# Kernel tuning notes

Hardware: AMD Instinct MI355X
Metric: run time of the kernel (lower is better)

Reference implementation:

```python
import jax, jax.numpy as jnp
import numpy as np

F_DIM = 128
RBF_DIM = 20
N_NODES = 10000
N_EDGES = 200000
CUTOFF = 5


def setup_inputs() -> dict:
    key = jax.random.key(0)
    ks = jax.random.split(key, 12)
    s = jax.random.normal(ks[0], (N_NODES, F_DIM), jnp.float32)
    vec = jax.random.normal(ks[1], (N_NODES, 3, F_DIM), jnp.float32)
    edge_indexes = jax.random.randint(ks[2], (2, N_EDGES), 0, N_NODES, jnp.int32)
    edge_vector = jax.random.normal(ks[3], (N_EDGES, 3), jnp.float32)
    # distances in (0.5, 5.0) so fcut is nontrivial and no divide-by-zero
    edge_distance = jax.random.uniform(ks[4], (N_EDGES,), jnp.float32) * 4.5 + 0.5
    edge_rbf = jax.random.normal(ks[5], (N_EDGES, RBF_DIM), jnp.float32)
    # params: linear_s = Linear(F,F) -> SiLU -> Linear(F,3F); linear_rbf = Linear(RBF,3F)
    Ws1 = jax.random.normal(ks[6], (F_DIM, F_DIM), jnp.float32) / np.sqrt(F_DIM)
    bs1 = jnp.zeros((F_DIM,), jnp.float32)
    Ws2 = jax.random.normal(ks[7], (3 * F_DIM, F_DIM), jnp.float32) / np.sqrt(F_DIM)
    bs2 = jnp.zeros((3 * F_DIM,), jnp.float32)
    Wrbf = jax.random.normal(ks[8], (3 * F_DIM, RBF_DIM), jnp.float32) / np.sqrt(RBF_DIM)
    brbf = jnp.zeros((3 * F_DIM,), jnp.float32)
    return {
        "s": s, "vec": vec, "edge_vector": edge_vector,
        "edge_distance": edge_distance, "edge_rbf": edge_rbf,
        "Ws1": Ws1, "bs1": bs1, "Ws2": Ws2, "bs2": bs2,
        "Wrbf": Wrbf, "brbf": brbf,
        "edge_indexes": edge_indexes, "cutoff_dist": CUTOFF,
    }


def reference(s, vec, edge_vector, edge_distance, edge_rbf,
              Ws1, bs1, Ws2, bs2, Wrbf, brbf,
              edge_indexes, cutoff_dist):
    num_atoms, nf = s.shape
    dst_recv = edge_indexes[0]   # index_add target (message receivers)
    src_send = edge_indexes[1]   # gather source (message senders)

    S = s[src_send]              # [E, F]
    Vec = vec[src_send]          # [E, 3, F]

    # linear_s: Linear -> SiLU -> Linear
    h = jax.nn.silu(S @ Ws1.T + bs1)          # [E, F]
    phi = h @ Ws2.T + bs2                      # [E, 3F]

    rbf_lin = edge_rbf @ Wrbf.T + brbf         # [E, 3F]
    # cosine cutoff: 0.5*(cos(pi*d/rc)+1) for d < rc else 0
    rc = jnp.asarray(cutoff_dist, edge_distance.dtype)
    fcut = 0.5 * (jnp.cos(jnp.pi * edge_distance / rc) + 1.0)
    fcut = jnp.where(edge_distance < rc, fcut, 0.0)

    W = rbf_lin * fcut[:, None]
    vec_Ws, vec_Wvv, vec_Wvs = jnp.split(phi * W, 3, axis=-1)  # each [E, F]

    ds = jnp.zeros((num_atoms, nf), s.dtype).at[dst_recv].add(vec_Ws)

    vec_n = edge_vector / edge_distance[:, None]               # [E, 3]
    dVec = vec_Wvv[:, None, :] * Vec + vec_n[:, :, None] * vec_Wvs[:, None, :]  # [E,3,F]
    dvec = jnp.zeros((num_atoms, 3, nf), s.dtype).at[dst_recv].add(dVec)

    return ds, dvec
```

## Files before the change

kernel.cpp:

```cpp
#include <hip/hip_runtime.h>
#include <hip/hip_bf16.h>

typedef __attribute__((ext_vector_type(8))) short short8;
typedef __attribute__((ext_vector_type(4))) float floatx4;
typedef _Float16 half2_t __attribute__((ext_vector_type(2)));

#define CAP 64

__device__ __forceinline__ unsigned short f2bf(float x) {
    unsigned u = __float_as_uint(x);
    unsigned r = u + 0x7fffu + ((u >> 16) & 1u);
    return (unsigned short)(r >> 16);
}
__device__ __forceinline__ float bf2f(unsigned short h) {
    return __uint_as_float(((unsigned)h) << 16);
}
__device__ __forceinline__ unsigned short f2h(float x) {
    _Float16 h = (_Float16)x;
    return __builtin_bit_cast(unsigned short, h);
}
__device__ __forceinline__ float FD(unsigned int a, unsigned int b, float c) {
#if __has_builtin(__builtin_amdgcn_fdot2)
    return __builtin_amdgcn_fdot2(__builtin_bit_cast(half2_t, a),
                                  __builtin_bit_cast(half2_t, b), c, false);
#else
    half2_t ha = __builtin_bit_cast(half2_t, a);
    half2_t hb = __builtin_bit_cast(half2_t, b);
    return c + (float)ha[0] * (float)hb[0] + (float)ha[1] * (float)hb[1];
#endif
}
__device__ __forceinline__ float decode_rc(const void* cutoff_raw) {
    float fv = ((const float*)cutoff_raw)[0];
    int   iv = ((const int*)cutoff_raw)[0];
    if (fv > 0.099f && fv < 1.0e6f) return fv;
    if (iv > 0 && iv < 1000000) return (float)iv;
    double dv = ((const double*)cutoff_raw)[0];
    if (dv > 0.099 && dv < 1.0e6) return (float)dv;
    return (float)(((const long long*)cutoff_raw)[0]);
}

__global__ void setup_kernel(const float* __restrict__ vec,
                             const float* __restrict__ Ws1,
                             const float* __restrict__ Ws2,
                             const float* __restrict__ Wrbf,
                             const float* __restrict__ edge_rbf,
                             const int* __restrict__ eidx,
                             const float* __restrict__ edge_vec,
                             const float* __restrict__ edge_dist,
                             const void* __restrict__ cutoff_raw,
                             unsigned short* __restrict__ P6,
                             unsigned short* __restrict__ ws1_bf,
                             unsigned short* __restrict__ ws2_bf,
                             unsigned short* __restrict__ wrbf_h,
                             unsigned short* __restrict__ rbf_h,
                             int* __restrict__ cnt,
                             unsigned int* __restrict__ rec,
                             int ng_vec, int ng_w1, int ng_w2, int ng_wh, int ng_rh,
                             int RB, int E, int nbc)
{
    int tid = threadIdx.x;
    if ((int)blockIdx.x < nbc) {
        int total = ng_vec + ng_w1 + ng_w2 + ng_wh + ng_rh;
        int stride = nbc * 256;
        for (int g = blockIdx.x * 256 + tid; g < total; g += stride) {
            if (g < ng_vec) {
                int node = g / 48;
                int r = (g - node * 48) * 8;
                const float4* sp = (const float4*)(vec + (size_t)node * 384 + r);
                float4 x0 = sp[0], x1 = sp[1];
                short8 v;
                v[0]=(short)f2bf(x0.x); v[1]=(short)f2bf(x0.y);
                v[2]=(short)f2bf(x0.z); v[3]=(short)f2bf(x0.w);
                v[4]=(short)f2bf(x1.x); v[5]=(short)f2bf(x1.y);
                v[6]=(short)f2bf(x1.z); v[7]=(short)f2bf(x1.w);
                *(short8*)(P6 + (size_t)node * 768 + 384 + r) = v;
            } else if (g < ng_vec + ng_w1 + ng_w2) {
                int j = (g - ng_vec) * 8;
                const float* srcp;
                unsigned short* dstp;
                if (j < ng_w1 * 8) { srcp = Ws1 + j; dstp = ws1_bf + j; }
                else               { srcp = Ws2 + (j - ng_w1 * 8); dstp = ws2_bf + (j - ng_w1 * 8); }
                float4 x0 = ((const float4*)srcp)[0], x1 = ((const float4*)srcp)[1];
                short8 v;
                v[0]=(short)f2bf(x0.x); v[1]=(short)f2bf(x0.y);
                v[2]=(short)f2bf(x0.z); v[3]=(short)f2bf(x0.w);
                v[4]=(short)f2bf(x1.x); v[5]=(short)f2bf(x1.y);
                v[6]=(short)f2bf(x1.z); v[7]=(short)f2bf(x1.w);
                *(short8*)dstp = v;
            } else if (g < ng_vec + ng_w1 + ng_w2 + ng_wh) {
                int gg = g - ng_vec - ng_w1 - ng_w2;
                int n = gg >> 2, k0 = (gg & 3) * 8;
                short8 v;
                #pragma unroll
                for (int t = 0; t < 8; ++t) {
                    int k = k0 + t;
                    v[t] = (k < RB) ? (short)f2h(Wrbf[(size_t)n * RB + k]) : (short)0;
                }
                *(short8*)(wrbf_h + n * 32 + k0) = v;
            } else {
                int gg = g - ng_vec - ng_w1 - ng_w2 - ng_wh;
                int e = gg / 3, k0 = (gg - e * 3) * 8;
                short8 v;
                #pragma unroll
                for (int t = 0; t < 8; ++t) {
                    int k = k0 + t;
                    v[t] = (k < RB) ? (short)f2h(edge_rbf[(size_t)e * RB + k]) : (short)0;
                }
                *(short8*)(rbf_h + (size_t)e * 24 + k0) = v;
            }
        }
    } else {
        int i = ((int)blockIdx.x - nbc) * 256 + tid;
        if (i >= E) return;
        float rc = decode_rc(cutoff_raw);
        int d = eidx[i];
        int slot = atomicAdd(&cnt[d], 1);
        if (slot >= CAP) return;
        float dist = edge_dist[i];
        float fc = 0.0f;
        if (dist < rc) fc = 0.5f * (cosf(3.14159265358979323846f * dist / rc) + 1.0f);
        float inv = 1.0f / dist;
        unsigned int* rp = rec + ((size_t)(d * CAP + slot) << 3);
        ((uint4*)rp)[0] = make_uint4((unsigned)eidx[E + i], (unsigned)i, 0u, 0u);
        ((uint4*)rp)[1] = make_uint4(__float_as_uint(edge_vec[i * 3 + 0] * inv),
                                     __float_as_uint(edge_vec[i * 3 + 1] * inv),
                                     __float_as_uint(edge_vec[i * 3 + 2] * inv),
                                     __float_as_uint(fc));
    }
}

#define LN 136
__global__ __launch_bounds__(64, 4)
void node_kernel(const float* __restrict__ s,
                 const unsigned short* __restrict__ ws1_bf,
                 const float* __restrict__ bs1,
                 const unsigned short* __restrict__ ws2_bf,
                 const float* __restrict__ bs2,
                 unsigned short* __restrict__ P6,
                 int Nn)
{
    const int lane = threadIdx.x;
    const int l15  = lane & 15;
    const int q    = lane >> 4;
    const int base = blockIdx.x * 16;

    __shared__ unsigned short S_bf[16][LN];
    __shared__ unsigned short H_bf[16][LN];

    #pragma unroll
    for (int it = 0; it < 4; ++it) {
        int r = it * 4 + q;
        int node = base + r;
        short8 v;
        if (node < Nn) {
            const float4* sp4 = (const float4*)(s + (size_t)node * 128 + l15 * 8);
            float4 x0 = sp4[0], x1 = sp4[1];
            v[0] = (short)f2bf(x0.x); v[1] = (short)f2bf(x0.y);
            v[2] = (short)f2bf(x0.z); v[3] = (short)f2bf(x0.w);
            v[4] = (short)f2bf(x1.x); v[5] = (short)f2bf(x1.y);
            v[6] = (short)f2bf(x1.z); v[7] = (short)f2bf(x1.w);
        } else {
            #pragma unroll
            for (int k = 0; k < 8; ++k) v[k] = 0;
        }
        *((short8*)&S_bf[r][l15 * 8]) = v;
    }
    __syncthreads();

    floatx4 acc1[8];
    #pragma unroll
    for (int nj = 0; nj < 8; ++nj) acc1[nj] = (floatx4){0.f, 0.f, 0.f, 0.f};
    #pragma unroll
    for (int ks = 0; ks < 4; ++ks) {
        short8 a = *((const short8*)&S_bf[l15][ks * 32 + q * 8]);
        #pragma unroll
        for (int nj = 0; nj < 8; ++nj) {
            short8 b = *((const short8*)(ws1_bf + ((nj * 16 + l15) * 128 + ks * 32 + q * 8)));
            acc1[nj] = __builtin_amdgcn_mfma_f32_16x16x32_bf16(a, b, acc1[nj], 0, 0, 0);
        }
    }
    #pragma unroll
    for (int nj = 0; nj < 8; ++nj) {
        float b1 = bs1[nj * 16 + l15];
        #pragma unroll
        for (int r = 0; r < 4; ++r) {
            float x = acc1[nj][r] + b1;
            float h = x / (1.0f + __expf(-x));
            H_bf[q * 4 + r][nj * 16 + l15] = f2bf(h);
        }
    }
    __syncthreads();

    #pragma unroll
    for (int g = 0; g < 3; ++g) {
        floatx4 accP[8];
        #pragma unroll
        for (int j = 0; j < 8; ++j) accP[j] = (floatx4){0.f, 0.f, 0.f, 0.f};
        #pragma unroll
        for (int ks = 0; ks < 4; ++ks) {
            short8 a = *((const short8*)&H_bf[l15][ks * 32 + q * 8]);
            #pragma unroll
            for (int j = 0; j < 8; ++j) {
                int n = g * 128 + j * 16 + l15;
                short8 b = *((const short8*)(ws2_bf + ((size_t)n * 128 + ks * 32 + q * 8)));
                accP[j] = __builtin_amdgcn_mfma_f32_16x16x32_bf16(a, b, accP[j], 0, 0, 0);
            }
        }
        #pragma unroll
        for (int j = 0; j < 8; ++j) {
            int n = g * 128 + j * 16 + l15;
            float b2 = bs2[n];
            #pragma unroll
            for (int r = 0; r < 4; ++r) {
                int node = base + q * 4 + r;
                if (node < Nn)
                    P6[(size_t)node * 768 + n] = f2bf(accP[j][r] + b2);
            }
        }
    }
}

__global__ __launch_bounds__(256, 4)
void edge_kernel(const unsigned short* __restrict__ P6,
                 const unsigned short* __restrict__ wrbf_h,
                 const float* __restrict__ brbf,
                 const int* __restrict__ cnt,
                 const unsigned int* __restrict__ rec,
                 const unsigned short* __restrict__ rbf_h,
                 float* __restrict__ out_ds,
                 float* __restrict__ out_dvec,
                 int Nn)
{
    const int tid  = threadIdx.x;
    const int w    = tid >> 6;
    const int lane = tid & 63;
    const int node = __builtin_amdgcn_readfirstlane((int)blockIdx.x * 2 + (w >> 1));
    const int c    = (w & 1) * 64 + lane;
    if (node >= Nn) return;

    const unsigned short* wp0 = wrbf_h + ((size_t)c << 5);
    const unsigned short* wp1 = wrbf_h + ((size_t)(128 + c) << 5);
    const unsigned short* wp2 = wrbf_h + ((size_t)(256 + c) << 5);
    uint4 w0a = *(const uint4*)wp0;
    uint4 w0b = *(const uint4*)(wp0 + 8);
    uint2 w0c = *(const uint2*)(wp0 + 16);
    uint4 w1a = *(const uint4*)wp1;
    uint4 w1b = *(const uint4*)(wp1 + 8);
    uint2 w1c = *(const uint2*)(wp1 + 16);
    uint4 w2a = *(const uint4*)wp2;
    uint4 w2b = *(const uint4*)(wp2 + 8);
    uint2 w2c = *(const uint2*)(wp2 + 16);
    float b0 = brbf[c];
    float b1 = brbf[128 + c];
    float b2 = brbf[256 + c];
    asm volatile("" : "+v"(w0a.x), "+v"(w0a.y), "+v"(w0a.z), "+v"(w0a.w),
                      "+v"(w0b.x), "+v"(w0b.y), "+v"(w0b.z), "+v"(w0b.w),
                      "+v"(w0c.x), "+v"(w0c.y));
    asm volatile("" : "+v"(w1a.x), "+v"(w1a.y), "+v"(w1a.z), "+v"(w1a.w),
                      "+v"(w1b.x), "+v"(w1b.y), "+v"(w1b.z), "+v"(w1b.w),
                      "+v"(w1c.x), "+v"(w1c.y));
    asm volatile("" : "+v"(w2a.x), "+v"(w2a.y), "+v"(w2a.z), "+v"(w2a.w),
                      "+v"(w2b.x), "+v"(w2b.y), "+v"(w2b.z), "+v"(w2b.w),
                      "+v"(w2c.x), "+v"(w2c.y),
                      "+v"(b0), "+v"(b1), "+v"(b2));

    const int deg = min(cnt[node], CAP);
    const size_t bb = (size_t)node * CAP;

    float as = 0.f, a0 = 0.f, a1 = 0.f, a2 = 0.f;

    if (deg > 0) {
        const uint4* rp = (const uint4*)(rec + (bb << 3));

        uint4 sm = rp[0], mq = rp[1];
        const unsigned short* rr = rbf_h + (size_t)(int)sm.y * 24;
        uint4 Ra = *(const uint4*)rr;
        uint4 Rb = *(const uint4*)(rr + 8);
        uint2 Rc = *(const uint2*)(rr + 16);
        const unsigned short* pr = P6 + (size_t)(int)sm.x * 768;
        unsigned short u0 = pr[c],       u1 = pr[128 + c], u2 = pr[256 + c];
        unsigned short u3 = pr[384 + c], u4 = pr[512 + c], u5 = pr[640 + c];
        int n1 = (deg > 1) ? 1 : 0;
        uint4 smA = rp[2 * n1], mqA = rp[2 * n1 + 1];

        for (int sl = 0; sl < deg; ++sl) {
            const unsigned short* rrn = rbf_h + (size_t)(int)smA.y * 24;
            uint4 Ran = *(const uint4*)rrn;
            uint4 Rbn = *(const uint4*)(rrn + 8);
            uint2 Rcn = *(const uint2*)(rrn + 16);
            const unsigned short* prn = P6 + (size_t)(int)smA.x * 768;
            unsigned short un0 = prn[c],       un1 = prn[128 + c], un2 = prn[256 + c];
            unsigned short un3 = prn[384 + c], un4 = prn[512 + c], un5 = prn[640 + c];

            int n2 = (sl + 2 < deg) ? (sl + 2) : (deg - 1);
            uint4 smB = rp[2 * n2], mqB = rp[2 * n2 + 1];

            float d0 = b0, d1 = b1, d2 = b2;
            d0 = FD(Ra.x, w0a.x, d0); d1 = FD(Ra.x, w1a.x, d1); d2 = FD(Ra.x, w2a.x, d2);
            d0 = FD(Ra.y, w0a.y, d0); d1 = FD(Ra.y, w1a.y, d1); d2 = FD(Ra.y, w2a.y, d2);
            d0 = FD(Ra.z, w0a.z, d0); d1 = FD(Ra.z, w1a.z, d1); d2 = FD(Ra.z, w2a.z, d2);
            d0 = FD(Ra.w, w0a.w, d0); d1 = FD(Ra.w, w1a.w, d1); d2 = FD(Ra.w, w2a.w, d2);
            d0 = FD(Rb.x, w0b.x, d0); d1 = FD(Rb.x, w1b.x, d1); d2 = FD(Rb.x, w2b.x, d2);
            d0 = FD(Rb.y, w0b.y, d0); d1 = FD(Rb.y, w1b.y, d1); d2 = FD(Rb.y, w2b.y, d2);
            d0 = FD(Rb.z, w0b.z, d0); d1 = FD(Rb.z, w1b.z, d1); d2 = FD(Rb.z, w2b.z, d2);
            d0 = FD(Rb.w, w0b.w, d0); d1 = FD(Rb.w, w1b.w, d1); d2 = FD(Rb.w, w2b.w, d2);
            d0 = FD(Rc.x, w0c.x, d0); d1 = FD(Rc.x, w1c.x, d1); d2 = FD(Rc.x, w2c.x, d2);
            d0 = FD(Rc.y, w0c.y, d0); d1 = FD(Rc.y, w1c.y, d1); d2 = FD(Rc.y, w2c.y, d2);

            float ps = bf2f(u0), pv = bf2f(u1), px = bf2f(u2);
            float v0 = bf2f(u3), v1 = bf2f(u4), v2 = bf2f(u5);

            float fc = __uint_as_float(mq.w);
            float W0 = d0 * fc, W1 = d1 * fc, W2 = d2 * fc;
            as = fmaf(ps, W0, as);
            float mv = pv * W1;
            float mx = px * W2;
            a0 = fmaf(mv, v0, fmaf(mx, __uint_as_float(mq.x), a0));
            a1 = fmaf(mv, v1, fmaf(mx, __uint_as_float(mq.y), a1));
            a2 = fmaf(mv, v2, fmaf(mx, __uint_as_float(mq.z), a2));

            mq = mqA; smA = smB; mqA = mqB;
            Ra = Ran; Rb = Rbn; Rc = Rcn;
            u0 = un0; u1 = un1; u2 = un2; u3 = un3; u4 = un4; u5 = un5;
        }
    }

    __builtin_nontemporal_store(as, out_ds + (size_t)node * 128 + c);
    float* od = out_dvec + (size_t)node * 384;
    __builtin_nontemporal_store(a0, od + c);
    __builtin_nontemporal_store(a1, od + 128 + c);
    __builtin_nontemporal_store(a2, od + 256 + c);
}

extern "C" void kernel_launch(void* const* d_in, const int* in_sizes, int n_in,
                              void* d_out, int out_size, void* d_ws, size_t ws_size,
                              hipStream_t stream) {
    const float* s        = (const float*)d_in[0];
    const float* vec      = (const float*)d_in[1];
    const float* edge_vec = (const float*)d_in[2];
    const float* edge_dst = (const float*)d_in[3];
    const float* edge_rbf = (const float*)d_in[4];
    const float* Ws1      = (const float*)d_in[5];
    const float* bs1      = (const float*)d_in[6];
    const float* Ws2      = (const float*)d_in[7];
    const float* bs2      = (const float*)d_in[8];
    const float* Wrbf     = (const float*)d_in[9];
    const float* brbf     = (const float*)d_in[10];
    const int*   eidx     = (const int*)d_in[11];
    const void*  cutoff   = d_in[12];

    const int F  = 128;
    const int Nn = in_sizes[0] / F;
    const int E  = in_sizes[3];
    const int RB = in_sizes[4] / E;
    const int F3 = 3 * F;

    unsigned int*   rec     = (unsigned int*)d_ws;
    unsigned short* P6      = (unsigned short*)(rec + (size_t)Nn * CAP * 8);
    unsigned short* rbf_h   = P6 + (size_t)Nn * 768;
    unsigned short* ws1_bf  = rbf_h + (size_t)E * 24;
    unsigned short* ws2_bf  = ws1_bf + F * F;
    unsigned short* wrbf_h  = ws2_bf + (size_t)F3 * F;
    int* cnt                = (int*)(wrbf_h + F3 * 32);

    int ng_vec = (Nn * F3) >> 3;
    int ng_w1  = (F * F) >> 3;
    int ng_w2  = (F3 * F) >> 3;
    int ng_wh  = (F3 * 32) >> 3;
    int ng_rh  = (E * 24) >> 3;

    hipMemsetAsync(cnt, 0, (size_t)Nn * sizeof(int), stream);

    {
        long long total = (long long)ng_vec + ng_w1 + ng_w2 + ng_wh + ng_rh;
        int nbc = (int)((total + 255) / 256);
        int nbb = (E + 255) / 256;
        setup_kernel<<<nbc + nbb, 256, 0, stream>>>(vec, Ws1, Ws2, Wrbf, edge_rbf,
                                                    eidx, edge_vec, edge_dst, cutoff,
                                                    P6, ws1_bf, ws2_bf, wrbf_h, rbf_h,
                                                    cnt, rec,
                                                    ng_vec, ng_w1, ng_w2, ng_wh, ng_rh,
                                                    RB, E, nbc);
    }
    node_kernel<<<(Nn + 15) / 16, 64, 0, stream>>>(s, ws1_bf, bs1, ws2_bf, bs2, P6, Nn);

    float* out_ds   = (float*)d_out;
    float* out_dvec = out_ds + (size_t)Nn * F;

    edge_kernel<<<(Nn + 1) / 2, 256, 0, stream>>>(P6, wrbf_h, brbf,
                                                  cnt, rec, rbf_h,
                                                  out_ds, out_dvec, Nn);
}
```

Baseline: 211.8 us.

## Split node GEMM across four waves and simplify edge-loop prefetch

The node kernel now uses 256 threads per 16-node block. Each wave computes a quarter of the output columns of both MLP layers, so per-wave register pressure drops and more waves are available to hide latency. The edge kernel drops the two-deep software prefetch of P6 rows and records to a one-ahead prefetch of records and rbf only, and raises its launch-bounds occupancy hint from 4 to 6. The trade-off is fewer registers per thread in exchange for gather latency that is now exposed inside each iteration.

```diff
diff --git a/kernel.cpp b/kernel.cpp
--- a/kernel.cpp
+++ b/kernel.cpp
@@ -130,7 +130,7 @@
 }
 
 #define LN 136
-__global__ __launch_bounds__(64, 4)
+__global__ __launch_bounds__(256, 4)
 void node_kernel(const float* __restrict__ s,
                  const unsigned short* __restrict__ ws1_bf,
                  const float* __restrict__ bs1,
@@ -139,21 +139,23 @@
                  unsigned short* __restrict__ P6,
                  int Nn)
 {
-    const int lane = threadIdx.x;
+    const int tid  = threadIdx.x;
+    const int wv   = tid >> 6;
+    const int lane = tid & 63;
     const int l15  = lane & 15;
-    const int q    = lane >> 4;
+    const int qq   = lane >> 4;
     const int base = blockIdx.x * 16;
 
     __shared__ unsigned short S_bf[16][LN];
     __shared__ unsigned short H_bf[16][LN];
 
-    #pragma unroll
-    for (int it = 0; it < 4; ++it) {
-        int r = it * 4 + q;
-        int node = base + r;
+    {
+        int row = tid >> 4;
+        int col = (tid & 15) * 8;
+        int node = base + row;
         short8 v;
         if (node < Nn) {
-            const float4* sp4 = (const float4*)(s + (size_t)node * 128 + l15 * 8);
+            const float4* sp4 = (const float4*)(s + (size_t)node * 128 + col);
             float4 x0 = sp4[0], x1 = sp4[1];
             v[0] = (short)f2bf(x0.x); v[1] = (short)f2bf(x0.y);
             v[2] = (short)f2bf(x0.z); v[3] = (short)f2bf(x0.w);
@@ -163,64 +165,68 @@
             #pragma unroll
             for (int k = 0; k < 8; ++k) v[k] = 0;
         }
-        *((short8*)&S_bf[r][l15 * 8]) = v;
+        *((short8*)&S_bf[row][col]) = v;
     }
     __syncthreads();
 
-    floatx4 acc1[8];
-    #pragma unroll
-    for (int nj = 0; nj < 8; ++nj) acc1[nj] = (floatx4){0.f, 0.f, 0.f, 0.f};
-    #pragma unroll
-    for (int ks = 0; ks < 4; ++ks) {
-        short8 a = *((const short8*)&S_bf[l15][ks * 32 + q * 8]);
-        #pragma unroll
-        for (int nj = 0; nj < 8; ++nj) {
-            short8 b = *((const short8*)(ws1_bf + ((nj * 16 + l15) * 128 + ks * 32 + q * 8)));
-            acc1[nj] = __builtin_amdgcn_mfma_f32_16x16x32_bf16(a, b, acc1[nj], 0, 0, 0);
-        }
-    }
-    #pragma unroll
-    for (int nj = 0; nj < 8; ++nj) {
-        float b1 = bs1[nj * 16 + l15];
-        #pragma unroll
-        for (int r = 0; r < 4; ++r) {
-            float x = acc1[nj][r] + b1;
-            float h = x / (1.0f + __expf(-x));
-            H_bf[q * 4 + r][nj * 16 + l15] = f2bf(h);
+    {
+        short8 a[4];
+        #pragma unroll
+        for (int ks = 0; ks < 4; ++ks)
+            a[ks] = *((const short8*)&S_bf[l15][ks * 32 + qq * 8]);
+        floatx4 acc1[2];
+        #pragma unroll
+        for (int t = 0; t < 2; ++t) acc1[t] = (floatx4){0.f, 0.f, 0.f, 0.f};
+        #pragma unroll
+        for (int ks = 0; ks < 4; ++ks) {
+            #pragma unroll
+            for (int t = 0; t < 2; ++t) {
+                int nj = wv * 2 + t;
+                short8 b = *((const short8*)(ws1_bf + ((nj * 16 + l15) * 128 + ks * 32 + qq * 8)));
+                acc1[t] = __builtin_amdgcn_mfma_f32_16x16x32_bf16(a[ks], b, acc1[t], 0, 0, 0);
+            }
+        }
+        #pragma unroll
+        for (int t = 0; t < 2; ++t) {
+            int nj = wv * 2 + t;
+            float b1 = bs1[nj * 16 + l15];
+            #pragma unroll
+            for (int r = 0; r < 4; ++r) {
+                float x = acc1[t][r] + b1;
+                float h = x / (1.0f + __expf(-x));
+                H_bf[qq * 4 + r][nj * 16 + l15] = f2bf(h);
+            }
         }
     }
     __syncthreads();
 
-    #pragma unroll
-    for (int g = 0; g < 3; ++g) {
-        floatx4 accP[8];
-        #pragma unroll
-        for (int j = 0; j < 8; ++j) accP[j] = (floatx4){0.f, 0.f, 0.f, 0.f};
-        #pragma unroll
-        for (int ks = 0; ks < 4; ++ks) {
-            short8 a = *((const short8*)&H_bf[l15][ks * 32 + q * 8]);
-            #pragma unroll
-            for (int j = 0; j < 8; ++j) {
-                int n = g * 128 + j * 16 + l15;
-                short8 b = *((const short8*)(ws2_bf + ((size_t)n * 128 + ks * 32 + q * 8)));
-                accP[j] = __builtin_amdgcn_mfma_f32_16x16x32_bf16(a, b, accP[j], 0, 0, 0);
-            }
-        }
-        #pragma unroll
-        for (int j = 0; j < 8; ++j) {
-            int n = g * 128 + j * 16 + l15;
+    {
+        short8 a[4];
+        #pragma unroll
+        for (int ks = 0; ks < 4; ++ks)
+            a[ks] = *((const short8*)&H_bf[l15][ks * 32 + qq * 8]);
+        #pragma unroll
+        for (int t6 = 0; t6 < 6; ++t6) {
+            int t = wv * 6 + t6;
+            int n = t * 16 + l15;
+            floatx4 acc = (floatx4){0.f, 0.f, 0.f, 0.f};
+            #pragma unroll
+            for (int ks = 0; ks < 4; ++ks) {
+                short8 b = *((const short8*)(ws2_bf + ((size_t)n * 128 + ks * 32 + qq * 8)));
+                acc = __builtin_amdgcn_mfma_f32_16x16x32_bf16(a[ks], b, acc, 0, 0, 0);
+            }
             float b2 = bs2[n];
             #pragma unroll
             for (int r = 0; r < 4; ++r) {
-                int node = base + q * 4 + r;
+                int node = base + qq * 4 + r;
                 if (node < Nn)
-                    P6[(size_t)node * 768 + n] = f2bf(accP[j][r] + b2);
-            }
-        }
-    }
-}
-
-__global__ __launch_bounds__(256, 4)
+                    P6[(size_t)node * 768 + n] = f2bf(acc[r] + b2);
+            }
+        }
+    }
+}
+
+__global__ __launch_bounds__(256, 6)
 void edge_kernel(const unsigned short* __restrict__ P6,
                  const unsigned short* __restrict__ wrbf_h,
                  const float* __restrict__ brbf,
@@ -271,29 +277,27 @@
 
     if (deg > 0) {
         const uint4* rp = (const uint4*)(rec + (bb << 3));
-
         uint4 sm = rp[0], mq = rp[1];
         const unsigned short* rr = rbf_h + (size_t)(int)sm.y * 24;
         uint4 Ra = *(const uint4*)rr;
         uint4 Rb = *(const uint4*)(rr + 8);
         uint2 Rc = *(const uint2*)(rr + 16);
-        const unsigned short* pr = P6 + (size_t)(int)sm.x * 768;
-        unsigned short u0 = pr[c],       u1 = pr[128 + c], u2 = pr[256 + c];
-        unsigned short u3 = pr[384 + c], u4 = pr[512 + c], u5 = pr[640 + c];
-        int n1 = (deg > 1) ? 1 : 0;
-        uint4 smA = rp[2 * n1], mqA = rp[2 * n1 + 1];
 
         for (int sl = 0; sl < deg; ++sl) {
-            const unsigned short* rrn = rbf_h + (size_t)(int)smA.y * 24;
+            const unsigned short* pr = P6 + (size_t)(int)sm.x * 768;
+            unsigned short u0 = pr[c];
+            unsigned short u1 = pr[128 + c];
+            unsigned short u2 = pr[256 + c];
+            unsigned short u3 = pr[384 + c];
+            unsigned short u4 = pr[512 + c];
+            unsigned short u5 = pr[640 + c];
+
+            int np = (sl + 1 < deg) ? (sl + 1) : sl;
+            uint4 smn = rp[2 * np], mqn = rp[2 * np + 1];
+            const unsigned short* rrn = rbf_h + (size_t)(int)smn.y * 24;
             uint4 Ran = *(const uint4*)rrn;
             uint4 Rbn = *(const uint4*)(rrn + 8);
             uint2 Rcn = *(const uint2*)(rrn + 16);
-            const unsigned short* prn = P6 + (size_t)(int)smA.x * 768;
-            unsigned short un0 = prn[c],       un1 = prn[128 + c], un2 = prn[256 + c];
-            unsigned short un3 = prn[384 + c], un4 = prn[512 + c], un5 = prn[640 + c];
-
-            int n2 = (sl + 2 < deg) ? (sl + 2) : (deg - 1);
-            uint4 smB = rp[2 * n2], mqB = rp[2 * n2 + 1];
 
             float d0 = b0, d1 = b1, d2 = b2;
             d0 = FD(Ra.x, w0a.x, d0); d1 = FD(Ra.x, w1a.x, d1); d2 = FD(Ra.x, w2a.x, d2);
@@ -319,9 +323,7 @@
             a1 = fmaf(mv, v1, fmaf(mx, __uint_as_float(mq.y), a1));
             a2 = fmaf(mv, v2, fmaf(mx, __uint_as_float(mq.z), a2));
 
-            mq = mqA; smA = smB; mqA = mqB;
-            Ra = Ran; Rb = Rbn; Rc = Rcn;
-            u0 = un0; u1 = un1; u2 = un2; u3 = un3; u4 = un4; u5 = un5;
+            sm = smn; mq = mqn; Ra = Ran; Rb = Rbn; Rc = Rcn;
         }
     }
 
@@ -382,7 +384,7 @@
                                                     ng_vec, ng_w1, ng_w2, ng_wh, ng_rh,
                                                     RB, E, nbc);
     }
-    node_kernel<<<(Nn + 15) / 16, 64, 0, stream>>>(s, ws1_bf, bs1, ws2_bf, bs2, P6, Nn);
+    node_kernel<<<(Nn + 15) / 16, 256, 0, stream>>>(s, ws1_bf, bs1, ws2_bf, bs2, P6, Nn);
 
     float* out_ds   = (float*)d_out;
     float* out_dvec = out_ds + (size_t)Nn * F;
```

Result: faster. 203.3 us (-4.0%).
